# Performance work log

Measured on AMD Instinct MI355X. Metric: run time of the kernel, lower is better.

## Reference

```python
import jax, jax.numpy as jnp
import numpy as np
from jax import lax

D_MODEL, D_STATE, D_CONV, N_BLOCKS = 128, 32, 8, 6
D_INNER, DT_RANK, K_PRE = 256, 8, 7  # expand=2, dt_rank=ceil(128/16)
BATCH, SEQ = 16, 4096


def setup_inputs() -> dict:
    key = jax.random.key(0)
    ks = jax.random.split(key, 16)
    def rn(k, shape, scale=0.05):
        return jax.random.normal(k, shape, jnp.float32) * scale
    return {
        "x": jax.random.normal(ks[0], (BATCH, SEQ, 1), jnp.float32),
        "pre_conv_w": rn(ks[1], (D_MODEL, 1, K_PRE), 0.3),
        "pre_conv_b": rn(ks[2], (D_MODEL,), 0.01),
        "in_proj_w": rn(ks[3], (N_BLOCKS, 2, 2 * D_INNER, D_MODEL)),
        "conv_w": rn(ks[4], (N_BLOCKS, 2, D_INNER, 1, D_CONV), 0.2),
        "conv_b": rn(ks[5], (N_BLOCKS, 2, D_INNER), 0.01),
        "x_proj_w": rn(ks[6], (N_BLOCKS, 2, DT_RANK + 2 * D_STATE, D_INNER)),
        "dt_proj_w": rn(ks[7], (N_BLOCKS, 2, D_INNER, DT_RANK), 0.1),
        "dt_proj_b": rn(ks[8], (N_BLOCKS, 2, D_INNER), 0.5),
        "A_log": jax.random.uniform(ks[9], (N_BLOCKS, 2, D_INNER, D_STATE), jnp.float32),
        "D_param": rn(ks[10], (N_BLOCKS, 2, D_INNER), 1.0),
        "out_proj_w": rn(ks[11], (N_BLOCKS, 2, D_MODEL, D_INNER)),
        "ln_g": jnp.ones((N_BLOCKS, D_MODEL), jnp.float32),
        "ln_b": jnp.zeros((N_BLOCKS, D_MODEL), jnp.float32),
        "proj_w": rn(ks[12], (1, D_MODEL), 0.1),
        "proj_b": jnp.zeros((1,), jnp.float32),
    }


def _layernorm(x, g, b, eps=1e-5):
    mu = jnp.mean(x, axis=-1, keepdims=True)
    var = jnp.mean(jnp.square(x - mu), axis=-1, keepdims=True)
    return (x - mu) * lax.rsqrt(var + eps) * g + b


def _mamba(x, in_w, cw, cb, xp_w, dt_w, dt_b, a_log, d_par, out_w):
    # x: [B, L, D_MODEL]
    B, L, _ = x.shape
    xz = jnp.einsum('bld,ed->ble', x, in_w)            # [B,L,2*D_INNER]
    u, z = xz[..., :D_INNER], xz[..., D_INNER:]
    # depthwise causal conv over time
    u = lax.conv_general_dilated(
        u.transpose(0, 2, 1), cw, (1,), [(D_CONV - 1, 0)],
        feature_group_count=D_INNER,
        dimension_numbers=('NCH', 'OIH', 'NCH')) + cb[None, :, None]
    u = jax.nn.silu(u).transpose(0, 2, 1)              # [B,L,D_INNER]
    dbc = jnp.einsum('bld,ed->ble', u, xp_w)           # [B,L,DT_RANK+2N]
    dt = jax.nn.softplus(jnp.einsum('blr,dr->bld', dbc[..., :DT_RANK], dt_w) + dt_b)
    Bm = dbc[..., DT_RANK:DT_RANK + D_STATE]           # [B,L,N]
    Cm = dbc[..., DT_RANK + D_STATE:]                  # [B,L,N]
    A = -jnp.exp(a_log)                                # [D_INNER,N]

    def step(h, inp):
        dt_t, B_t, C_t, u_t = inp                      # [B,d],[B,n],[B,n],[B,d]
        dA = jnp.exp(dt_t[..., None] * A)              # [B,d,n]
        h = h * dA + (dt_t * u_t)[..., None] * B_t[:, None, :]
        y = jnp.einsum('bdn,bn->bd', h, C_t)
        return h, y

    h0 = jnp.zeros((B, D_INNER, D_STATE), x.dtype)
    _, ys = lax.scan(step, h0, (dt.transpose(1, 0, 2), Bm.transpose(1, 0, 2),
                                Cm.transpose(1, 0, 2), u.transpose(1, 0, 2)))
    y = ys.transpose(1, 0, 2) + u * d_par              # [B,L,D_INNER]
    y = y * jax.nn.silu(z)
    return jnp.einsum('ble,de->bld', y, out_w)         # [B,L,D_MODEL]


def reference(x, pre_conv_w, pre_conv_b, in_proj_w, conv_w, conv_b, x_proj_w,
              dt_proj_w, dt_proj_b, A_log, D_param, out_proj_w, ln_g, ln_b,
              proj_w, proj_b):
    pad = K_PRE // 2
    h = lax.conv_general_dilated(
        x.transpose(0, 2, 1), pre_conv_w, (1,), [(pad, pad)],
        dimension_numbers=('NCH', 'OIH', 'NCH')) + pre_conv_b[None, :, None]
    h = jax.nn.gelu(h, approximate=False).transpose(0, 2, 1)  # [B,L,D_MODEL]
    for i in range(N_BLOCKS):
        f = _mamba(h, in_proj_w[i, 0], conv_w[i, 0], conv_b[i, 0], x_proj_w[i, 0],
                   dt_proj_w[i, 0], dt_proj_b[i, 0], A_log[i, 0], D_param[i, 0],
                   out_proj_w[i, 0])
        hb = jnp.flip(h, axis=1)
        b = _mamba(hb, in_proj_w[i, 1], conv_w[i, 1], conv_b[i, 1], x_proj_w[i, 1],
                   dt_proj_w[i, 1], dt_proj_b[i, 1], A_log[i, 1], D_param[i, 1],
                   out_proj_w[i, 1])
        b = jnp.flip(b, axis=1)
        out = (f + b) * 0.5
        h = _layernorm(out + h, ln_g[i], ln_b[i])  # dropout: eval mode (identity)
    y = jnp.einsum('bld,od->blo', h, proj_w) + proj_b
    return y[..., 0]  # [B, L]
```

## Files before the change

### kernel.cpp

```cpp
#include <hip/hip_runtime.h>
#include <hip/hip_bf16.h>
#include <cstdint>
#include <cstddef>

#define L_SEQ   4096
#define BATCH_N 16
#define BLTOK   (BATCH_N * L_SEQ)
#define DMODEL  128
#define DINNER  256
#define DSTATE  32
#define DTRANK  8

#define LC  64
#define GCH 64
#define LOG2E 1.44269504088896340736f

typedef _Float16 half8 __attribute__((ext_vector_type(8)));
typedef float    floatx4 __attribute__((ext_vector_type(4)));

#define LDSW 40

__global__ __launch_bounds__(128) void pre_conv_gelu(
    const float* __restrict__ x,
    const float* __restrict__ w,
    const float* __restrict__ bias,
    float* __restrict__ h,
    _Float16* __restrict__ hb)
{
    int r = blockIdx.x;
    int c = threadIdx.x;
    int b = r >> 12;
    int l = r & 4095;
    float acc = bias[c];
    const float* wp = w + c * 7;
#pragma unroll
    for (int k = 0; k < 7; ++k) {
        int ll = l + k - 3;
        if (ll >= 0 && ll < L_SEQ)
            acc += x[(size_t)(b << 12) + ll] * wp[k];
    }
    float ge = 0.5f * acc * (1.f + erff(acc * 0.70710678118654752f));
    h[(size_t)r * DMODEL + c]  = ge;
    hb[(size_t)r * DMODEL + c] = (_Float16)ge;
}

__global__ __launch_bounds__(256) void cvt_weights(
    const float* __restrict__ inw,  _Float16* __restrict__ inwh,
    const float* __restrict__ xpw,  _Float16* __restrict__ xpwh,
    const float* __restrict__ outw, _Float16* __restrict__ outwh)
{
    int i = blockIdx.x * 256 + threadIdx.x;
    if (i < 12 * 512 * 128) inwh[i]  = (_Float16)inw[i];
    if (i < 12 * 72 * 256)  xpwh[i]  = (_Float16)xpw[i];
    if (i < 12 * 128 * 256) outwh[i] = (_Float16)outw[i];
}

__global__ __launch_bounds__(256) void gemm_mfma(
    const _Float16* __restrict__ A, int lda,
    const _Float16* __restrict__ W, int ldw,
    float* __restrict__ Out,
    _Float16* __restrict__ U16,
    __hip_bfloat16* __restrict__ Zb,
    int N, int K, int rev, int mode)
{
    __shared__ __align__(16) _Float16 As[64 * LDSW];
    __shared__ __align__(16) _Float16 Ws[64 * LDSW];

    int tid  = threadIdx.x;
    int wave = tid >> 6;
    int lane = tid & 63;
    int m0 = blockIdx.y * 64;
    int n0 = blockIdx.x * 64;

    int srow = tid >> 2;
    int skc  = (tid & 3) * 8;

    int garow = m0 + srow;
    if (rev) { int bb = garow >> 12; int ll = garow & 4095; garow = (bb << 12) + (4095 - ll); }
    const _Float16* Aptr = A + (size_t)garow * lda + skc;
    int wrow = n0 + srow;
    bool wok = (wrow < N);
    const _Float16* Wptr = W + (size_t)(wok ? wrow : 0) * ldw + skc;

    int lr = lane & 15;
    int lk = (lane >> 4) * 8;
    int soff = srow * LDSW + skc;
    int aoff = (16 * wave + lr) * LDSW + lk;

    floatx4 acc0 = {0.f, 0.f, 0.f, 0.f};
    floatx4 acc1 = acc0, acc2 = acc0, acc3 = acc0;

    for (int k0 = 0; k0 < K; k0 += 32) {
        half8 av = *(const half8*)(Aptr + k0);
        half8 bv = {};
        if (wok) bv = *(const half8*)(Wptr + k0);
        __syncthreads();
        *(half8*)&As[soff] = av;
        *(half8*)&Ws[soff] = bv;
        __syncthreads();
        half8 af = *(const half8*)&As[aoff];
        half8 b0 = *(const half8*)&Ws[( 0 + lr) * LDSW + lk];
        half8 b1 = *(const half8*)&Ws[(16 + lr) * LDSW + lk];
        half8 b2 = *(const half8*)&Ws[(32 + lr) * LDSW + lk];
        half8 b3 = *(const half8*)&Ws[(48 + lr) * LDSW + lk];
        acc0 = __builtin_amdgcn_mfma_f32_16x16x32_f16(af, b0, acc0, 0, 0, 0);
        acc1 = __builtin_amdgcn_mfma_f32_16x16x32_f16(af, b1, acc1, 0, 0, 0);
        acc2 = __builtin_amdgcn_mfma_f32_16x16x32_f16(af, b2, acc2, 0, 0, 0);
        acc3 = __builtin_amdgcn_mfma_f32_16x16x32_f16(af, b3, acc3, 0, 0, 0);
    }

    int orow = m0 + 16 * wave + (lane >> 4) * 4;
    floatx4 av4[4] = {acc0, acc1, acc2, acc3};
#pragma unroll
    for (int jb = 0; jb < 4; ++jb) {
        int col = n0 + jb * 16 + lr;
#pragma unroll
        for (int r = 0; r < 4; ++r) {
            int row = orow + r;
            float v = av4[jb][r];
            if (mode == 0) {
                if (col < N) Out[(size_t)row * 72 + col] = v;
            } else if (mode == 1) {
                if (col < 256) U16[(size_t)row * 256 + col] = (_Float16)v;
                else Zb[(size_t)row * 256 + (col - 256)] = __float2bfloat16(v);
            } else if (mode == 2) {
                U16[(size_t)row * 128 + col] = (_Float16)v;
            } else {
                int bb = row >> 12, ll = row & 4095;
                size_t o = ((size_t)(bb << 12) + (4095 - ll)) * 128 + col;
                U16[o] = (_Float16)(0.5f * ((float)U16[o] + v));
            }
        }
    }
}

__global__ __launch_bounds__(256) void dwconv_silu(
    const _Float16* __restrict__ u,
    const float* __restrict__ cw,
    const float* __restrict__ cb,
    _Float16* __restrict__ uc)
{
    int b  = blockIdx.x >> 7;
    int lt = blockIdx.x & 127;
    int l0 = lt * 32;
    int d  = threadIdx.x;

    float wv[8];
    const float* wp = cw + d * 8;
#pragma unroll
    for (int k = 0; k < 8; ++k) wv[k] = wp[k];
    float bias = cb[d];

    size_t rowb = (size_t)(b << 12);
    float win[8];
#pragma unroll
    for (int j = 0; j < 7; ++j) {
        int ll = l0 - 7 + j;
        win[j] = (ll >= 0) ? (float)u[(rowb + ll) * DINNER + d] : 0.f;
    }
#pragma unroll
    for (int i = 0; i < 32; ++i) {
        int l = l0 + i;
        win[7] = (float)u[(rowb + l) * DINNER + d];
        float acc = bias;
#pragma unroll
        for (int j = 0; j < 8; ++j) acc += win[j] * wv[j];
        float s = acc / (1.f + __expf(-acc));
        uc[(rowb + l) * DINNER + d] = (_Float16)s;
#pragma unroll
        for (int j = 0; j < 7; ++j) win[j] = win[j + 1];
    }
}

__global__ __launch_bounds__(256, 4) void scan_phase1(
    const float* __restrict__ dbc,
    const _Float16* __restrict__ u,
    float* __restrict__ aggh,
    float* __restrict__ aggs,
    const float* __restrict__ dt_w,
    const float* __restrict__ dt_b,
    const float* __restrict__ a_log)
{
    __shared__ __align__(16) float sh[LC * 72];
    int bg = blockIdx.x;
    int b  = bg >> 6;
    int g  = bg & (GCH - 1);
    int d  = threadIdx.x;

    size_t base = (size_t)b * L_SEQ + (size_t)g * LC;
    {
        const float4* src4 = (const float4*)(dbc + base * 72);
        float4* dst4 = (float4*)sh;
        for (int i = d; i < LC * 18; i += 256) dst4[i] = src4[i];
    }

    const float* wr = dt_w + d * DTRANK;
    float w0 = wr[0], w1 = wr[1], w2 = wr[2], w3 = wr[3];
    float w4 = wr[4], w5 = wr[5], w6 = wr[6], w7 = wr[7];
    float bias = dt_b[d];

    float al2[32];
    {
        const float4* ar = (const float4*)(a_log + d * DSTATE);
#pragma unroll
        for (int k = 0; k < 8; ++k) {
            float4 v = ar[k];
            al2[4 * k + 0] = -__expf(v.x) * LOG2E;
            al2[4 * k + 1] = -__expf(v.y) * LOG2E;
            al2[4 * k + 2] = -__expf(v.z) * LOG2E;
            al2[4 * k + 3] = -__expf(v.w) * LOG2E;
        }
    }
    __syncthreads();

    float h[32];
#pragma unroll
    for (int n = 0; n < 32; ++n) h[n] = 0.f;
    float S = 0.f;

    for (int t = 0; t < LC; ++t) {
        const float* row = sh + t * 72;
        float4 r0 = *(const float4*)row;
        float4 r1 = *(const float4*)(row + 4);
        float dtr = bias + r0.x * w0 + r0.y * w1 + r0.z * w2 + r0.w * w3
                         + r1.x * w4 + r1.y * w5 + r1.z * w6 + r1.w * w7;
        float dtv = (dtr > 15.f) ? dtr : __logf(1.f + __expf(dtr));
        S += dtv;
        float du = dtv * (float)u[(base + t) * DINNER + d];
#pragma unroll
        for (int n = 0; n < 32; n += 4) {
            float4 Bv = *(const float4*)(row + 8 + n);
            h[n + 0] = h[n + 0] * __builtin_amdgcn_exp2f(dtv * al2[n + 0]) + du * Bv.x;
            h[n + 1] = h[n + 1] * __builtin_amdgcn_exp2f(dtv * al2[n + 1]) + du * Bv.y;
            h[n + 2] = h[n + 2] * __builtin_amdgcn_exp2f(dtv * al2[n + 2]) + du * Bv.z;
            h[n + 3] = h[n + 3] * __builtin_amdgcn_exp2f(dtv * al2[n + 3]) + du * Bv.w;
        }
    }

    size_t ob = ((size_t)(b * GCH + g) * 32) * 256 + d;
#pragma unroll
    for (int n = 0; n < 32; ++n) aggh[ob + (size_t)n * 256] = h[n];
    aggs[(size_t)(b * GCH + g) * 256 + d] = S;
}

__global__ __launch_bounds__(256) void scan_phase2(
    float* __restrict__ aggh,
    const float* __restrict__ aggs,
    const float* __restrict__ a_log)
{
    int b = blockIdx.x >> 5;
    int n = blockIdx.x & 31;
    int d = threadIdx.x;

    float a = -__expf(a_log[d * DSTATE + n]);
    float hrun = 0.f;
    for (int g = 0; g < GCH; ++g) {
        size_t os = (size_t)(b * GCH + g) * 256 + d;
        size_t oh = ((size_t)(b * GCH + g) * 32 + n) * 256 + d;
        float S  = aggs[os];
        float he = aggh[oh];
        aggh[oh] = hrun;
        hrun = hrun * __expf(a * S) + he;
    }
}

__global__ __launch_bounds__(256, 4) void scan_phase3(
    const float* __restrict__ dbc,
    const _Float16* __restrict__ u,
    const __hip_bfloat16* __restrict__ z_in,
    _Float16* __restrict__ y_out,
    const float* __restrict__ aggh,
    const float* __restrict__ dt_w,
    const float* __restrict__ dt_b,
    const float* __restrict__ a_log,
    const float* __restrict__ Dp)
{
    __shared__ __align__(16) float sh[LC * 72];
    int bg = blockIdx.x;
    int b  = bg >> 6;
    int g  = bg & (GCH - 1);
    int d  = threadIdx.x;

    size_t base = (size_t)b * L_SEQ + (size_t)g * LC;
    {
        const float4* src4 = (const float4*)(dbc + base * 72);
        float4* dst4 = (float4*)sh;
        for (int i = d; i < LC * 18; i += 256) dst4[i] = src4[i];
    }

    const float* wr = dt_w + d * DTRANK;
    float w0 = wr[0], w1 = wr[1], w2 = wr[2], w3 = wr[3];
    float w4 = wr[4], w5 = wr[5], w6 = wr[6], w7 = wr[7];
    float bias = dt_b[d];
    float Dd = Dp[d];

    float al2[32];
    {
        const float4* ar = (const float4*)(a_log + d * DSTATE);
#pragma unroll
        for (int k = 0; k < 8; ++k) {
            float4 v = ar[k];
            al2[4 * k + 0] = -__expf(v.x) * LOG2E;
            al2[4 * k + 1] = -__expf(v.y) * LOG2E;
            al2[4 * k + 2] = -__expf(v.z) * LOG2E;
            al2[4 * k + 3] = -__expf(v.w) * LOG2E;
        }
    }

    float h[32];
    size_t ob = ((size_t)(b * GCH + g) * 32) * 256 + d;
#pragma unroll
    for (int n = 0; n < 32; ++n) h[n] = aggh[ob + (size_t)n * 256];

    __syncthreads();

    for (int t = 0; t < LC; ++t) {
        const float* row = sh + t * 72;
        float4 r0 = *(const float4*)row;
        float4 r1 = *(const float4*)(row + 4);
        float dtr = bias + r0.x * w0 + r0.y * w1 + r0.z * w2 + r0.w * w3
                         + r1.x * w4 + r1.y * w5 + r1.z * w6 + r1.w * w7;
        float dtv = (dtr > 15.f) ? dtr : __logf(1.f + __expf(dtr));
        float uv = (float)u[(base + t) * DINNER + d];
        float du = dtv * uv;
        float zv = __bfloat162float(z_in[(base + t) * DINNER + d]);

        float y = 0.f;
#pragma unroll
        for (int n = 0; n < 32; n += 4) {
            float4 Bv = *(const float4*)(row + 8 + n);
            float4 Cv = *(const float4*)(row + 40 + n);
            h[n + 0] = h[n + 0] * __builtin_amdgcn_exp2f(dtv * al2[n + 0]) + du * Bv.x;
            h[n + 1] = h[n + 1] * __builtin_amdgcn_exp2f(dtv * al2[n + 1]) + du * Bv.y;
            h[n + 2] = h[n + 2] * __builtin_amdgcn_exp2f(dtv * al2[n + 2]) + du * Bv.z;
            h[n + 3] = h[n + 3] * __builtin_amdgcn_exp2f(dtv * al2[n + 3]) + du * Bv.w;
            y += h[n + 0] * Cv.x + h[n + 1] * Cv.y
               + h[n + 2] * Cv.z + h[n + 3] * Cv.w;
        }
        float yv = y + uv * Dd;
        float sig = 1.f / (1.f + __expf(-zv));
        y_out[(base + t) * DINNER + d] = (_Float16)(yv * (zv * sig));
    }
}

__global__ __launch_bounds__(128) void combine_ln(
    const _Float16* __restrict__ osum,
    float* __restrict__ h,
    _Float16* __restrict__ hb,
    const float* __restrict__ g,
    const float* __restrict__ be)
{
    __shared__ float red[128];
    int r = blockIdx.x;
    int c = threadIdx.x;
    size_t idx = (size_t)r * DMODEL + c;

    float v = (float)osum[idx] + h[idx];

    red[c] = v;
    __syncthreads();
    for (int s = 64; s > 0; s >>= 1) {
        if (c < s) red[c] += red[c + s];
        __syncthreads();
    }
    float mu = red[0] * (1.f / 128.f);
    __syncthreads();
    float dv = v - mu;
    red[c] = dv * dv;
    __syncthreads();
    for (int s = 64; s > 0; s >>= 1) {
        if (c < s) red[c] += red[c + s];
        __syncthreads();
    }
    float var = red[0] * (1.f / 128.f);
    float o = dv * rsqrtf(var + 1e-5f) * g[c] + be[c];
    h[idx]  = o;
    hb[idx] = (_Float16)o;
}

__global__ __launch_bounds__(128) void final_proj(
    const float* __restrict__ h,
    const float* __restrict__ pw,
    const float* __restrict__ pb,
    float* __restrict__ out)
{
    __shared__ float red[128];
    int r = blockIdx.x;
    int c = threadIdx.x;
    red[c] = h[(size_t)r * DMODEL + c] * pw[c];
    __syncthreads();
    for (int s = 64; s > 0; s >>= 1) {
        if (c < s) red[c] += red[c + s];
        __syncthreads();
    }
    if (c == 0) out[r] = red[0] + pb[0];
}

extern "C" void kernel_launch(void* const* d_in, const int* in_sizes, int n_in,
                              void* d_out, int out_size, void* d_ws, size_t ws_size,
                              hipStream_t stream)
{
    const float* x    = (const float*)d_in[0];
    const float* pcw  = (const float*)d_in[1];
    const float* pcb  = (const float*)d_in[2];
    const float* inw  = (const float*)d_in[3];
    const float* cw   = (const float*)d_in[4];
    const float* cb   = (const float*)d_in[5];
    const float* xpw  = (const float*)d_in[6];
    const float* dtw  = (const float*)d_in[7];
    const float* dtb  = (const float*)d_in[8];
    const float* alog = (const float*)d_in[9];
    const float* dpar = (const float*)d_in[10];
    const float* outw = (const float*)d_in[11];
    const float* lng  = (const float*)d_in[12];
    const float* lnb  = (const float*)d_in[13];
    const float* pw   = (const float*)d_in[14];
    const float* pb   = (const float*)d_in[15];
    float* out = (float*)d_out;

    float* h  = (float*)d_ws;
    float* A  = h + (size_t)BLTOK * 128;
    __hip_bfloat16* zy = (__hip_bfloat16*)(A + (size_t)BLTOK * 256);
    _Float16* ucb = (_Float16*)((char*)zy + (size_t)BLTOK * 256 * 2);
    _Float16* hb  = (_Float16*)((char*)ucb + (size_t)BLTOK * 256 * 2);
    _Float16* E16 = (_Float16*)((char*)hb + (size_t)BLTOK * 128 * 2);
    _Float16* inwh  = E16 + (size_t)BLTOK * 128;
    _Float16* xpwh  = inwh + (size_t)12 * 512 * 128;
    _Float16* outwh = xpwh + (size_t)12 * 72 * 256;
    float* aggs = (float*)(outwh + (size_t)12 * 128 * 256);
    _Float16* u16 = (_Float16*)A;
    float* dbc  = A;
    float* aggh = A + (size_t)BLTOK * 128;

    cvt_weights<<<(12 * 512 * 128 + 255) / 256, 256, 0, stream>>>(
        inw, inwh, xpw, xpwh, outw, outwh);
    pre_conv_gelu<<<BLTOK, 128, 0, stream>>>(x, pcw, pcb, h, hb);

    for (int blk = 0; blk < 6; ++blk) {
        for (int dir = 0; dir < 2; ++dir) {
            int s = blk * 2 + dir;
            gemm_mfma<<<dim3(8, BLTOK / 64), 256, 0, stream>>>(
                hb, DMODEL, inwh + (size_t)s * 512 * 128, 128,
                nullptr, u16, zy, 512, 128, dir, 1);
            dwconv_silu<<<16 * 128, 256, 0, stream>>>(
                u16, cw + (size_t)s * 256 * 8, cb + (size_t)s * 256, ucb);
            gemm_mfma<<<dim3(2, BLTOK / 64), 256, 0, stream>>>(
                ucb, DINNER, xpwh + (size_t)s * 72 * 256, 256,
                dbc, nullptr, nullptr, 72, 256, 0, 0);
            scan_phase1<<<16 * GCH, 256, 0, stream>>>(
                dbc, ucb, aggh, aggs,
                dtw + (size_t)s * 256 * 8, dtb + (size_t)s * 256,
                alog + (size_t)s * 256 * 32);
            scan_phase2<<<16 * 32, 256, 0, stream>>>(
                aggh, aggs, alog + (size_t)s * 256 * 32);
            scan_phase3<<<16 * GCH, 256, 0, stream>>>(
                dbc, ucb, zy, (_Float16*)zy, aggh,
                dtw + (size_t)s * 256 * 8, dtb + (size_t)s * 256,
                alog + (size_t)s * 256 * 32, dpar + (size_t)s * 256);
            gemm_mfma<<<dim3(2, BLTOK / 64), 256, 0, stream>>>(
                (const _Float16*)zy, DINNER, outwh + (size_t)s * 128 * 256, 256,
                nullptr, E16, nullptr, 128, 256, 0, 2 + dir);
        }
        combine_ln<<<BLTOK, 128, 0, stream>>>(
            E16, h, hb, lng + blk * 128, lnb + blk * 128);
    }

    final_proj<<<BLTOK, 128, 0, stream>>>(h, pw, pb, out);
}
```

Baseline: 4.401 ms.

## Compute chunk-local scan output in phase1 and replace phase3 with additive correction

The first scan pass now produces the zero-initial-state output y0 per chunk, writes it back over the u buffer along with the running cumulative dt sum, and stores chunk-end states in fp16. The third pass no longer re-runs the recurrence. It adds a correction exp(cumdt*A)·h_in·C to y0 and applies the SiLU(z) gate, which removes the second serial 32-state recurrence. In exchange, each element costs an extra fp16 read and write of cumdt and y0. Storing aggregated states and cumulative sums in fp16 may lose accuracy over long chunks.

```diff
diff --git a/kernel.cpp b/kernel.cpp
--- a/kernel.cpp
+++ b/kernel.cpp
@@ -174,12 +174,14 @@
 
 __global__ __launch_bounds__(256, 4) void scan_phase1(
     const float* __restrict__ dbc,
-    const _Float16* __restrict__ u,
-    float* __restrict__ aggh,
+    _Float16* ucy,
+    _Float16* __restrict__ cums,
+    _Float16* __restrict__ aggh,
     float* __restrict__ aggs,
     const float* __restrict__ dt_w,
     const float* __restrict__ dt_b,
-    const float* __restrict__ a_log)
+    const float* __restrict__ a_log,
+    const float* __restrict__ Dp)
 {
     __shared__ __align__(16) float sh[LC * 72];
     int bg = blockIdx.x;
@@ -198,6 +200,7 @@
     float w0 = wr[0], w1 = wr[1], w2 = wr[2], w3 = wr[3];
     float w4 = wr[4], w5 = wr[5], w6 = wr[6], w7 = wr[7];
     float bias = dt_b[d];
+    float Dd = Dp[d];
 
     float al2[32];
     {
@@ -226,104 +229,8 @@
                          + r1.x * w4 + r1.y * w5 + r1.z * w6 + r1.w * w7;
         float dtv = (dtr > 15.f) ? dtr : __logf(1.f + __expf(dtr));
         S += dtv;
-        float du = dtv * (float)u[(base + t) * DINNER + d];
-#pragma unroll
-        for (int n = 0; n < 32; n += 4) {
-            float4 Bv = *(const float4*)(row + 8 + n);
-            h[n + 0] = h[n + 0] * __builtin_amdgcn_exp2f(dtv * al2[n + 0]) + du * Bv.x;
-            h[n + 1] = h[n + 1] * __builtin_amdgcn_exp2f(dtv * al2[n + 1]) + du * Bv.y;
-            h[n + 2] = h[n + 2] * __builtin_amdgcn_exp2f(dtv * al2[n + 2]) + du * Bv.z;
-            h[n + 3] = h[n + 3] * __builtin_amdgcn_exp2f(dtv * al2[n + 3]) + du * Bv.w;
-        }
-    }
-
-    size_t ob = ((size_t)(b * GCH + g) * 32) * 256 + d;
-#pragma unroll
-    for (int n = 0; n < 32; ++n) aggh[ob + (size_t)n * 256] = h[n];
-    aggs[(size_t)(b * GCH + g) * 256 + d] = S;
-}
-
-__global__ __launch_bounds__(256) void scan_phase2(
-    float* __restrict__ aggh,
-    const float* __restrict__ aggs,
-    const float* __restrict__ a_log)
-{
-    int b = blockIdx.x >> 5;
-    int n = blockIdx.x & 31;
-    int d = threadIdx.x;
-
-    float a = -__expf(a_log[d * DSTATE + n]);
-    float hrun = 0.f;
-    for (int g = 0; g < GCH; ++g) {
-        size_t os = (size_t)(b * GCH + g) * 256 + d;
-        size_t oh = ((size_t)(b * GCH + g) * 32 + n) * 256 + d;
-        float S  = aggs[os];
-        float he = aggh[oh];
-        aggh[oh] = hrun;
-        hrun = hrun * __expf(a * S) + he;
-    }
-}
-
-__global__ __launch_bounds__(256, 4) void scan_phase3(
-    const float* __restrict__ dbc,
-    const _Float16* __restrict__ u,
-    const __hip_bfloat16* __restrict__ z_in,
-    _Float16* __restrict__ y_out,
-    const float* __restrict__ aggh,
-    const float* __restrict__ dt_w,
-    const float* __restrict__ dt_b,
-    const float* __restrict__ a_log,
-    const float* __restrict__ Dp)
-{
-    __shared__ __align__(16) float sh[LC * 72];
-    int bg = blockIdx.x;
-    int b  = bg >> 6;
-    int g  = bg & (GCH - 1);
-    int d  = threadIdx.x;
-
-    size_t base = (size_t)b * L_SEQ + (size_t)g * LC;
-    {
-        const float4* src4 = (const float4*)(dbc + base * 72);
-        float4* dst4 = (float4*)sh;
-        for (int i = d; i < LC * 18; i += 256) dst4[i] = src4[i];
-    }
-
-    const float* wr = dt_w + d * DTRANK;
-    float w0 = wr[0], w1 = wr[1], w2 = wr[2], w3 = wr[3];
-    float w4 = wr[4], w5 = wr[5], w6 = wr[6], w7 = wr[7];
-    float bias = dt_b[d];
-    float Dd = Dp[d];
-
-    float al2[32];
-    {
-        const float4* ar = (const float4*)(a_log + d * DSTATE);
-#pragma unroll
-        for (int k = 0; k < 8; ++k) {
-            float4 v = ar[k];
-            al2[4 * k + 0] = -__expf(v.x) * LOG2E;
-            al2[4 * k + 1] = -__expf(v.y) * LOG2E;
-            al2[4 * k + 2] = -__expf(v.z) * LOG2E;
-            al2[4 * k + 3] = -__expf(v.w) * LOG2E;
-        }
-    }
-
-    float h[32];
-    size_t ob = ((size_t)(b * GCH + g) * 32) * 256 + d;
-#pragma unroll
-    for (int n = 0; n < 32; ++n) h[n] = aggh[ob + (size_t)n * 256];
-
-    __syncthreads();
-
-    for (int t = 0; t < LC; ++t) {
-        const float* row = sh + t * 72;
-        float4 r0 = *(const float4*)row;
-        float4 r1 = *(const float4*)(row + 4);
-        float dtr = bias + r0.x * w0 + r0.y * w1 + r0.z * w2 + r0.w * w3
-                         + r1.x * w4 + r1.y * w5 + r1.z * w6 + r1.w * w7;
-        float dtv = (dtr > 15.f) ? dtr : __logf(1.f + __expf(dtr));
-        float uv = (float)u[(base + t) * DINNER + d];
+        float uv = (float)ucy[(base + t) * DINNER + d];
         float du = dtv * uv;
-        float zv = __bfloat162float(z_in[(base + t) * DINNER + d]);
 
         float y = 0.f;
 #pragma unroll
@@ -337,9 +244,101 @@
             y += h[n + 0] * Cv.x + h[n + 1] * Cv.y
                + h[n + 2] * Cv.z + h[n + 3] * Cv.w;
         }
-        float yv = y + uv * Dd;
+        ucy[(base + t) * DINNER + d]  = (_Float16)(y + uv * Dd);
+        cums[(base + t) * DINNER + d] = (_Float16)S;
+    }
+
+    size_t ob = ((size_t)(b * GCH + g) * 32) * 256 + d;
+#pragma unroll
+    for (int n = 0; n < 32; ++n) aggh[ob + (size_t)n * 256] = (_Float16)h[n];
+    aggs[(size_t)(b * GCH + g) * 256 + d] = S;
+}
+
+__global__ __launch_bounds__(256) void scan_phase2(
+    _Float16* __restrict__ aggh,
+    const float* __restrict__ aggs,
+    const float* __restrict__ a_log)
+{
+    int b = blockIdx.x >> 5;
+    int n = blockIdx.x & 31;
+    int d = threadIdx.x;
+
+    float a = -__expf(a_log[d * DSTATE + n]);
+    float hrun = 0.f;
+    for (int g = 0; g < GCH; ++g) {
+        size_t os = (size_t)(b * GCH + g) * 256 + d;
+        size_t oh = ((size_t)(b * GCH + g) * 32 + n) * 256 + d;
+        float S  = aggs[os];
+        float he = (float)aggh[oh];
+        aggh[oh] = (_Float16)hrun;
+        hrun = hrun * __expf(a * S) + he;
+    }
+}
+
+__global__ __launch_bounds__(256, 4) void scan_corr(
+    const float* __restrict__ dbc,
+    const _Float16* __restrict__ y0,
+    const _Float16* __restrict__ cums,
+    const __hip_bfloat16* __restrict__ z_in,
+    _Float16* __restrict__ y_out,
+    const _Float16* __restrict__ aggh,
+    const float* __restrict__ a_log)
+{
+    __shared__ __align__(16) float shc[LC * 32];
+    int bg = blockIdx.x;
+    int b  = bg >> 6;
+    int g  = bg & (GCH - 1);
+    int d  = threadIdx.x;
+
+    size_t base = (size_t)b * L_SEQ + (size_t)g * LC;
+    {
+        const float4* src4 = (const float4*)(dbc + base * 72);
+        float4* dst4 = (float4*)shc;
+        for (int i = d; i < LC * 8; i += 256) {
+            int t = i >> 3, q = i & 7;
+            dst4[t * 8 + q] = src4[t * 18 + 10 + q];
+        }
+    }
+
+    float al2[32];
+    {
+        const float4* ar = (const float4*)(a_log + d * DSTATE);
+#pragma unroll
+        for (int k = 0; k < 8; ++k) {
+            float4 v = ar[k];
+            al2[4 * k + 0] = -__expf(v.x) * LOG2E;
+            al2[4 * k + 1] = -__expf(v.y) * LOG2E;
+            al2[4 * k + 2] = -__expf(v.z) * LOG2E;
+            al2[4 * k + 3] = -__expf(v.w) * LOG2E;
+        }
+    }
+
+    float hin[32];
+    size_t ob = ((size_t)(b * GCH + g) * 32) * 256 + d;
+#pragma unroll
+    for (int n = 0; n < 32; ++n) hin[n] = (float)aggh[ob + (size_t)n * 256];
+
+    __syncthreads();
+
+    for (int t = 0; t < LC; ++t) {
+        size_t idx = (base + t) * DINNER + d;
+        float cs  = (float)cums[idx];
+        float y0v = (float)y0[idx];
+        float zv  = __bfloat162float(z_in[idx]);
+        const float* Crow = shc + t * 32;
+
+        float corr = 0.f;
+#pragma unroll
+        for (int n = 0; n < 32; n += 4) {
+            float4 Cv = *(const float4*)(Crow + n);
+            corr += __builtin_amdgcn_exp2f(cs * al2[n + 0]) * hin[n + 0] * Cv.x;
+            corr += __builtin_amdgcn_exp2f(cs * al2[n + 1]) * hin[n + 1] * Cv.y;
+            corr += __builtin_amdgcn_exp2f(cs * al2[n + 2]) * hin[n + 2] * Cv.z;
+            corr += __builtin_amdgcn_exp2f(cs * al2[n + 3]) * hin[n + 3] * Cv.w;
+        }
+        float yv = y0v + corr;
         float sig = 1.f / (1.f + __expf(-zv));
-        y_out[(base + t) * DINNER + d] = (_Float16)(yv * (zv * sig));
+        y_out[idx] = (_Float16)(yv * (zv * sig));
     }
 }
 
@@ -419,18 +418,19 @@
     float* out = (float*)d_out;
 
     float* h  = (float*)d_ws;
-    float* A  = h + (size_t)BLTOK * 128;
-    __hip_bfloat16* zy = (__hip_bfloat16*)(A + (size_t)BLTOK * 256);
+    _Float16* A16 = (_Float16*)(h + (size_t)BLTOK * 128);
+    _Float16* u16 = A16;
+    float* dbc = (float*)A16;
+    __hip_bfloat16* zy = (__hip_bfloat16*)(A16 + (size_t)BLTOK * 256);
     _Float16* ucb = (_Float16*)((char*)zy + (size_t)BLTOK * 256 * 2);
-    _Float16* hb  = (_Float16*)((char*)ucb + (size_t)BLTOK * 256 * 2);
-    _Float16* E16 = (_Float16*)((char*)hb + (size_t)BLTOK * 128 * 2);
+    _Float16* hb  = ucb + (size_t)BLTOK * 256;
+    _Float16* E16 = hb + (size_t)BLTOK * 128;
     _Float16* inwh  = E16 + (size_t)BLTOK * 128;
     _Float16* xpwh  = inwh + (size_t)12 * 512 * 128;
     _Float16* outwh = xpwh + (size_t)12 * 72 * 256;
     float* aggs = (float*)(outwh + (size_t)12 * 128 * 256);
-    _Float16* u16 = (_Float16*)A;
-    float* dbc  = A;
-    float* aggh = A + (size_t)BLTOK * 128;
+    _Float16* aggh = (_Float16*)(aggs + (size_t)16 * GCH * 256);
+    _Float16* cums = aggh + (size_t)16 * GCH * 32 * 256;
 
     cvt_weights<<<(12 * 512 * 128 + 255) / 256, 256, 0, stream>>>(
         inw, inwh, xpw, xpwh, outw, outwh);
@@ -448,15 +448,14 @@
                 ucb, DINNER, xpwh + (size_t)s * 72 * 256, 256,
                 dbc, nullptr, nullptr, 72, 256, 0, 0);
             scan_phase1<<<16 * GCH, 256, 0, stream>>>(
-                dbc, ucb, aggh, aggs,
+                dbc, ucb, cums, aggh, aggs,
                 dtw + (size_t)s * 256 * 8, dtb + (size_t)s * 256,
-                alog + (size_t)s * 256 * 32);
+                alog + (size_t)s * 256 * 32, dpar + (size_t)s * 256);
             scan_phase2<<<16 * 32, 256, 0, stream>>>(
                 aggh, aggs, alog + (size_t)s * 256 * 32);
-            scan_phase3<<<16 * GCH, 256, 0, stream>>>(
-                dbc, ucb, zy, (_Float16*)zy, aggh,
-                dtw + (size_t)s * 256 * 8, dtb + (size_t)s * 256,
-                alog + (size_t)s * 256 * 32, dpar + (size_t)s * 256);
+            scan_corr<<<16 * GCH, 256, 0, stream>>>(
+                dbc, ucb, cums, zy, (_Float16*)zy, aggh,
+                alog + (size_t)s * 256 * 32);
             gemm_mfma<<<dim3(2, BLTOK / 64), 256, 0, stream>>>(
                 (const _Float16*)zy, DINNER, outwh + (size_t)s * 128 * 256, 256,
                 nullptr, E16, nullptr, 128, 256, 0, 2 + dir);
```

After: 4.221 ms. 1.04x faster.
